# Kernel optimization log

Measured on AMD Instinct MI355X. Metric: run time of the kernel, lower is better.

Reference implementation:

```python
import jax, jax.numpy as jnp
import numpy as np

B = 4096        # batch size
IN = 4096       # in_size
P = 16          # n_partitions
E = IN // P     # embed_dim = 256
EPS = 1e-5
SCALE = np.float32(np.sqrt(E))


def setup_inputs() -> dict:
    key = jax.random.key(0)
    ks = jax.random.split(key, 8)
    rn = lambda k, shape, s=1.0: jax.random.normal(k, shape, dtype=jnp.float32) * s
    return {
        "x": rn(ks[0], (B, IN)),
        "gamma": jnp.ones((IN,), jnp.float32),   # BatchNorm weight
        "beta": jnp.zeros((IN,), jnp.float32),   # BatchNorm bias
        "WQ": rn(ks[1], (E, E), 0.05), "bQ": rn(ks[2], (E,), 0.05),
        "WK": rn(ks[3], (E, E), 0.05), "bK": rn(ks[4], (E,), 0.05),
        "WV": rn(ks[5], (E, E), 0.05), "bV": rn(ks[6], (E,), 0.05),
    }


def reference(x, gamma, beta, WQ, bQ, WK, bK, WV, bV):
    # Training-mode BatchNorm1d over the batch dim (computed once; the torch
    # loop recomputes the identical result n_partitions*3 times).
    mean = jnp.mean(x, axis=0)
    var = jnp.var(x, axis=0)  # biased, as torch BN uses for normalization
    xn = (x - mean) * jax.lax.rsqrt(var + EPS) * gamma + beta

    # Split features into P partitions of size E; shared projections per partition.
    xr = xn.reshape(B, P, E)                      # partition i -> xr[:, i, :]
    Q = xr @ WQ.T + bQ                            # (B, P, E); torch Q[b,e,p] = Q[b,p,e]
    K = xr @ WK.T + bK                            # (B, P, E)
    V = xr @ WV.T + bV                            # (B, P, E)

    # bmm(Q, K^T) with torch layout (B,E,P) x (B,P,E) -> (B,E,E)
    scores = jnp.einsum('bpe,bpf->bef', Q, K) / SCALE
    attn = jax.nn.softmax(scores, axis=2)         # Softmax(dim=2)
    prod = jnp.einsum('bef,bpf->bep', attn, V)    # (B, E, P)

    # torch.cat over embed_dim rows == row-major reshape of (E,P)
    out = prod.reshape(B, E * P) + x
    return out
```

## Files before the change

kernel.cpp:

```cpp
#include <hip/hip_runtime.h>
#include <hip/hip_bf16.h>

#define B_SZ   4096
#define IN_SZ  4096
#define EPS_F  1e-5f
#define CEXP   0.09016844005555896f

typedef __bf16 bf16x8 __attribute__((ext_vector_type(8)));
typedef float  f32x4  __attribute__((ext_vector_type(4)));
typedef float  f32x16 __attribute__((ext_vector_type(16)));

static __device__ __forceinline__ unsigned short f2bf(float f) {
    union { float f; unsigned int u; } c; c.f = f;
    unsigned int u = c.u;
    return (unsigned short)((u + 0x7FFFu + ((u >> 16) & 1u)) >> 16);
}
static __device__ __forceinline__ unsigned short bfbits(float f) {
    __bf16 h = (__bf16)f;
    return __builtin_bit_cast(unsigned short, h);
}
static __device__ __forceinline__ unsigned int pk2(float a, float b) {
    return (unsigned int)bfbits(a) | ((unsigned int)bfbits(b) << 16);
}

__global__ __launch_bounds__(256) void stats_kernel(const float* __restrict__ x,
                                                    float* __restrict__ colsum,
                                                    float* __restrict__ colsq) {
    int c4 = blockIdx.x * 256 + threadIdx.x;
    int r0 = blockIdx.y * 64;
    float4 s = {0.f, 0.f, 0.f, 0.f}, q = {0.f, 0.f, 0.f, 0.f};
    const float4* p = reinterpret_cast<const float4*>(x) + (size_t)r0 * 1024 + c4;
    #pragma unroll 4
    for (int r = 0; r < 64; ++r) {
        float4 v = p[(size_t)r * 1024];
        s.x += v.x; s.y += v.y; s.z += v.z; s.w += v.w;
        q.x += v.x * v.x; q.y += v.y * v.y; q.z += v.z * v.z; q.w += v.w * v.w;
    }
    int j = c4 * 4;
    atomicAdd(&colsum[j + 0], s.x); atomicAdd(&colsum[j + 1], s.y);
    atomicAdd(&colsum[j + 2], s.z); atomicAdd(&colsum[j + 3], s.w);
    atomicAdd(&colsq[j + 0], q.x);  atomicAdd(&colsq[j + 1], q.y);
    atomicAdd(&colsq[j + 2], q.z);  atomicAdd(&colsq[j + 3], q.w);
}

__global__ __launch_bounds__(256) void prep_kernel(const float* __restrict__ gamma,
                                                   const float* __restrict__ beta,
                                                   const float* __restrict__ WQ,
                                                   const float* __restrict__ WK,
                                                   const float* __restrict__ WV,
                                                   const float* __restrict__ colsum,
                                                   const float* __restrict__ colsq,
                                                   float* __restrict__ scale,
                                                   float* __restrict__ shift,
                                                   unsigned short* __restrict__ wbf) {
    int i = blockIdx.x * 256 + threadIdx.x;
    if (i < IN_SZ) {
        float mean = colsum[i] * (1.0f / B_SZ);
        float var  = colsq[i] * (1.0f / B_SZ) - mean * mean;
        float sc   = gamma[i] * rsqrtf(var + EPS_F);
        scale[i] = sc;
        shift[i] = beta[i] - mean * sc;
    }
    wbf[i]           = f2bf(WQ[i]);
    wbf[65536 + i]   = f2bf(WK[i]);
    wbf[131072 + i]  = f2bf(WV[i]);
}

__global__ __launch_bounds__(256, 3) void attn3_kernel(
    const float* __restrict__ x,
    const float* __restrict__ scale,
    const float* __restrict__ shift,
    const unsigned short* __restrict__ wbf,
    const float* __restrict__ bQ,
    const float* __restrict__ bK,
    const float* __restrict__ bV,
    float* __restrict__ out)
{
    __shared__ __align__(16) unsigned short smem[25728];

    const int tid  = threadIdx.x;
    const int lane = tid & 63;
    const int w    = tid >> 6;
    const int b    = blockIdx.x;

    unsigned short* qT  = smem;
    unsigned short* kT  = smem + 6144;
    unsigned short* vS  = smem + 12288;
    unsigned short* xr  = smem + 16512;
    unsigned short* att = smem + 16512 + w * 2304;

    const float* xb = x + (size_t)b * IN_SZ;

    for (int i = tid; i < IN_SZ / 4; i += 256) {
        float4 xv = reinterpret_cast<const float4*>(xb)[i];
        float4 sc = reinterpret_cast<const float4*>(scale)[i];
        float4 sh = reinterpret_cast<const float4*>(shift)[i];
        int j = i * 4;
        int p = j >> 8, f = j & 255;
        unsigned int lo = pk2(xv.x * sc.x + sh.x, xv.y * sc.y + sh.y);
        unsigned int hi = pk2(xv.z * sc.z + sh.z, xv.w * sc.w + sh.w);
        *reinterpret_cast<uint2*>(&xr[p * 264 + f]) = make_uint2(lo, hi);
    }
    __syncthreads();

    const int r16 = lane & 15;
    const int g4  = lane >> 4;
    for (int t = w; t < 48; t += 4) {
        int proj = t >> 4;
        int et   = t & 15;
        const unsigned short* Wg = wbf + proj * 65536 + (et * 16 + r16) * 256 + 8 * g4;
        const unsigned short* arow = &xr[r16 * 264 + 8 * g4];
        f32x4 acc = {0.f, 0.f, 0.f, 0.f};
        #pragma unroll
        for (int kt = 0; kt < 8; ++kt) {
            bf16x8 av = *reinterpret_cast<const bf16x8*>(arow + 32 * kt);
            bf16x8 bv = *reinterpret_cast<const bf16x8*>(Wg + 32 * kt);
            acc = __builtin_amdgcn_mfma_f32_16x16x32_bf16(av, bv, acc, 0, 0, 0);
        }
        const float* bias = (proj == 0) ? bQ : (proj == 1) ? bK : bV;
        float bvv = bias[et * 16 + r16];
        if (proj < 2) {
            unsigned short* dst = (proj == 0 ? qT : kT) + (et * 16 + r16) * 24 + 4 * g4;
            *reinterpret_cast<uint2*>(dst) =
                make_uint2(pk2(acc[0] + bvv, acc[1] + bvv), pk2(acc[2] + bvv, acc[3] + bvv));
        } else {
            #pragma unroll
            for (int i = 0; i < 4; ++i)
                vS[(4 * g4 + i) * 264 + et * 16 + r16] = bfbits(acc[i] + bvv);
        }
    }
    __syncthreads();

    const int c32  = lane & 31;
    const int hi32 = lane >> 5;
    float* ob = out + (size_t)b * IN_SZ;

    for (int et2 = w; et2 < 8; et2 += 4) {
        int e0 = et2 * 32;
        bf16x8 qfrag = *reinterpret_cast<const bf16x8*>(&qT[(e0 + c32) * 24 + 8 * hi32]);
        f32x4 o0 = {0.f, 0.f, 0.f, 0.f}, o1 = {0.f, 0.f, 0.f, 0.f};
        float sum = 0.f;

        #pragma unroll
        for (int fb = 0; fb < 4; ++fb) {
            #pragma unroll
            for (int dd = 0; dd < 2; ++dd) {
                int d = 2 * fb + dd;
                bf16x8 kfrag = *reinterpret_cast<const bf16x8*>(&kT[(32 * d + c32) * 24 + 8 * hi32]);
                f32x16 s;
                #pragma unroll
                for (int r = 0; r < 16; ++r) s[r] = 0.f;
                s = __builtin_amdgcn_mfma_f32_32x32x16_bf16(kfrag, qfrag, s, 0, 0, 0);
                #pragma unroll
                for (int q = 0; q < 4; ++q) {
                    float p0 = exp2f(s[4*q+0] * CEXP);
                    float p1 = exp2f(s[4*q+1] * CEXP);
                    float p2 = exp2f(s[4*q+2] * CEXP);
                    float p3 = exp2f(s[4*q+3] * CEXP);
                    sum += (p0 + p1) + (p2 + p3);
                    *reinterpret_cast<uint2*>(&att[c32 * 72 + dd * 32 + 8 * q + 4 * hi32]) =
                        make_uint2(pk2(p0, p1), pk2(p2, p3));
                }
            }
            #pragma unroll
            for (int kt = 0; kt < 2; ++kt) {
                int fo = 64 * fb + 32 * kt + 8 * g4;
                bf16x8 vfr = *reinterpret_cast<const bf16x8*>(&vS[r16 * 264 + fo]);
                bf16x8 a0  = *reinterpret_cast<const bf16x8*>(&att[r16 * 72 + 32 * kt + 8 * g4]);
                o0 = __builtin_amdgcn_mfma_f32_16x16x32_bf16(a0, vfr, o0, 0, 0, 0);
                bf16x8 a1  = *reinterpret_cast<const bf16x8*>(&att[(16 + r16) * 72 + 32 * kt + 8 * g4]);
                o1 = __builtin_amdgcn_mfma_f32_16x16x32_bf16(a1, vfr, o1, 0, 0, 0);
            }
        }

        sum += __shfl_xor(sum, 32, 64);
        float rinv = 1.0f / sum;
        #pragma unroll
        for (int r = 0; r < 4; ++r) {
            float ri0 = __shfl(rinv, 4 * g4 + r, 64);
            float ri1 = __shfl(rinv, 16 + 4 * g4 + r, 64);
            int j0 = (e0 + 4 * g4 + r) * 16 + r16;
            int j1 = (e0 + 16 + 4 * g4 + r) * 16 + r16;
            ob[j0] = o0[r] * ri0 + xb[j0];
            ob[j1] = o1[r] * ri1 + xb[j1];
        }
    }
}

extern "C" void kernel_launch(void* const* d_in, const int* in_sizes, int n_in,
                              void* d_out, int out_size, void* d_ws, size_t ws_size,
                              hipStream_t stream) {
    (void)in_sizes; (void)n_in; (void)out_size; (void)ws_size;
    const float* x     = (const float*)d_in[0];
    const float* gamma = (const float*)d_in[1];
    const float* beta  = (const float*)d_in[2];
    const float* WQ    = (const float*)d_in[3];
    const float* bQv   = (const float*)d_in[4];
    const float* WK    = (const float*)d_in[5];
    const float* bKv   = (const float*)d_in[6];
    const float* WV    = (const float*)d_in[7];
    const float* bVv   = (const float*)d_in[8];
    float* out = (float*)d_out;

    float* colsum = (float*)d_ws;
    float* colsq  = colsum + 4096;
    float* scale  = colsum + 8192;
    float* shift  = colsum + 12288;
    unsigned short* wbf = (unsigned short*)(colsum + 16384);

    hipMemsetAsync(colsum, 0, 8192 * sizeof(float), stream);
    stats_kernel<<<dim3(4, 64), 256, 0, stream>>>(x, colsum, colsq);
    prep_kernel<<<256, 256, 0, stream>>>(gamma, beta, WQ, WK, WV, colsum, colsq, scale, shift, wbf);
    attn3_kernel<<<4096, 256, 0, stream>>>(x, scale, shift, wbf, bQv, bKv, bVv, out);
}
```

Before: 334.5 us.

## Keep normalized input in registers, swizzle LDS layouts, raise occupancy, fast exp2

Each wave now normalizes its x fragment straight from global memory into registers for the projection MFMAs, so the xr staging buffer in LDS and one barrier go away. The padded LDS layouts for Q, K, V and the attention tile are replaced by dense buffers with XOR swizzles. This shrinks shared memory to 40 KB, allowing launch bounds of 4 blocks per CU. exp2f is also swapped for the hardware exp2 builtin. In exchange, every wave reloads x, scale and shift redundantly (the 4 waves duplicate the same loads), and register pressure is higher under the tighter launch bound.

```diff
diff --git a/kernel.cpp b/kernel.cpp
--- a/kernel.cpp
+++ b/kernel.cpp
@@ -9,6 +9,12 @@
 typedef __bf16 bf16x8 __attribute__((ext_vector_type(8)));
 typedef float  f32x4  __attribute__((ext_vector_type(4)));
 typedef float  f32x16 __attribute__((ext_vector_type(16)));
+
+#if __has_builtin(__builtin_amdgcn_exp2f)
+#define FAST_EXP2(x) __builtin_amdgcn_exp2f(x)
+#else
+#define FAST_EXP2(x) exp2f(x)
+#endif
 
 static __device__ __forceinline__ unsigned short f2bf(float f) {
     union { float f; unsigned int u; } c; c.f = f;
@@ -66,7 +72,7 @@
     wbf[131072 + i]  = f2bf(WV[i]);
 }
 
-__global__ __launch_bounds__(256, 3) void attn3_kernel(
+__global__ __launch_bounds__(256, 4) void attn4_kernel(
     const float* __restrict__ x,
     const float* __restrict__ scale,
     const float* __restrict__ shift,
@@ -76,57 +82,72 @@
     const float* __restrict__ bV,
     float* __restrict__ out)
 {
-    __shared__ __align__(16) unsigned short smem[25728];
+    __shared__ __align__(16) unsigned short smem[20480];
+    char* const base = reinterpret_cast<char*>(smem);
 
     const int tid  = threadIdx.x;
     const int lane = tid & 63;
     const int w    = tid >> 6;
     const int b    = blockIdx.x;
-
-    unsigned short* qT  = smem;
-    unsigned short* kT  = smem + 6144;
-    unsigned short* vS  = smem + 12288;
-    unsigned short* xr  = smem + 16512;
-    unsigned short* att = smem + 16512 + w * 2304;
+    const int r16  = lane & 15;
+    const int g4   = lane >> 4;
+
+    char* const qT  = base;
+    char* const kT  = base + 8192;
+    char* const vS  = base + 16384;
+    char* const att = base + 24576 + w * 4096;
 
     const float* xb = x + (size_t)b * IN_SZ;
 
-    for (int i = tid; i < IN_SZ / 4; i += 256) {
-        float4 xv = reinterpret_cast<const float4*>(xb)[i];
-        float4 sc = reinterpret_cast<const float4*>(scale)[i];
-        float4 sh = reinterpret_cast<const float4*>(shift)[i];
-        int j = i * 4;
-        int p = j >> 8, f = j & 255;
-        unsigned int lo = pk2(xv.x * sc.x + sh.x, xv.y * sc.y + sh.y);
-        unsigned int hi = pk2(xv.z * sc.z + sh.z, xv.w * sc.w + sh.w);
-        *reinterpret_cast<uint2*>(&xr[p * 264 + f]) = make_uint2(lo, hi);
-    }
-    __syncthreads();
-
-    const int r16 = lane & 15;
-    const int g4  = lane >> 4;
+    bf16x8 areg[8];
+    {
+        const float* xr  = xb    + r16 * 256;
+        const float* scr = scale + r16 * 256;
+        const float* shr = shift + r16 * 256;
+        #pragma unroll
+        for (int kt = 0; kt < 8; ++kt) {
+            int c = 8 * g4 + 32 * kt;
+            float4 x0 = *reinterpret_cast<const float4*>(xr + c);
+            float4 x1 = *reinterpret_cast<const float4*>(xr + c + 4);
+            float4 s0 = *reinterpret_cast<const float4*>(scr + c);
+            float4 s1 = *reinterpret_cast<const float4*>(scr + c + 4);
+            float4 h0 = *reinterpret_cast<const float4*>(shr + c);
+            float4 h1 = *reinterpret_cast<const float4*>(shr + c + 4);
+            union { bf16x8 v; unsigned int u[4]; } t;
+            t.u[0] = pk2(fmaf(x0.x, s0.x, h0.x), fmaf(x0.y, s0.y, h0.y));
+            t.u[1] = pk2(fmaf(x0.z, s0.z, h0.z), fmaf(x0.w, s0.w, h0.w));
+            t.u[2] = pk2(fmaf(x1.x, s1.x, h1.x), fmaf(x1.y, s1.y, h1.y));
+            t.u[3] = pk2(fmaf(x1.z, s1.z, h1.z), fmaf(x1.w, s1.w, h1.w));
+            areg[kt] = t.v;
+        }
+    }
+
     for (int t = w; t < 48; t += 4) {
         int proj = t >> 4;
         int et   = t & 15;
         const unsigned short* Wg = wbf + proj * 65536 + (et * 16 + r16) * 256 + 8 * g4;
-        const unsigned short* arow = &xr[r16 * 264 + 8 * g4];
         f32x4 acc = {0.f, 0.f, 0.f, 0.f};
         #pragma unroll
         for (int kt = 0; kt < 8; ++kt) {
-            bf16x8 av = *reinterpret_cast<const bf16x8*>(arow + 32 * kt);
             bf16x8 bv = *reinterpret_cast<const bf16x8*>(Wg + 32 * kt);
-            acc = __builtin_amdgcn_mfma_f32_16x16x32_bf16(av, bv, acc, 0, 0, 0);
+            acc = __builtin_amdgcn_mfma_f32_16x16x32_bf16(areg[kt], bv, acc, 0, 0, 0);
         }
         const float* bias = (proj == 0) ? bQ : (proj == 1) ? bK : bV;
         float bvv = bias[et * 16 + r16];
         if (proj < 2) {
-            unsigned short* dst = (proj == 0 ? qT : kT) + (et * 16 + r16) * 24 + 4 * g4;
-            *reinterpret_cast<uint2*>(dst) =
+            int e = et * 16 + r16;
+            unsigned off = (unsigned)(e * 32 + 8 * g4);
+            off ^= ((off >> 7) & 1u) << 4;
+            *reinterpret_cast<uint2*>((proj == 0 ? qT : kT) + off) =
                 make_uint2(pk2(acc[0] + bvv, acc[1] + bvv), pk2(acc[2] + bvv, acc[3] + bvv));
         } else {
             #pragma unroll
-            for (int i = 0; i < 4; ++i)
-                vS[(4 * g4 + i) * 264 + et * 16 + r16] = bfbits(acc[i] + bvv);
+            for (int i = 0; i < 4; ++i) {
+                int p = 4 * g4 + i;
+                unsigned off = (unsigned)(p * 512 + (et * 16 + r16) * 2);
+                off ^= ((off >> 9) & 7u) << 4;
+                *reinterpret_cast<unsigned short*>(vS + off) = bfbits(acc[i] + bvv);
+            }
         }
     }
     __syncthreads();
@@ -137,7 +158,9 @@
 
     for (int et2 = w; et2 < 8; et2 += 4) {
         int e0 = et2 * 32;
-        bf16x8 qfrag = *reinterpret_cast<const bf16x8*>(&qT[(e0 + c32) * 24 + 8 * hi32]);
+        unsigned qoff = (unsigned)((e0 + c32) * 32 + 16 * hi32);
+        qoff ^= ((qoff >> 7) & 1u) << 4;
+        bf16x8 qfrag = *reinterpret_cast<const bf16x8*>(qT + qoff);
         f32x4 o0 = {0.f, 0.f, 0.f, 0.f}, o1 = {0.f, 0.f, 0.f, 0.f};
         float sum = 0.f;
 
@@ -146,29 +169,37 @@
             #pragma unroll
             for (int dd = 0; dd < 2; ++dd) {
                 int d = 2 * fb + dd;
-                bf16x8 kfrag = *reinterpret_cast<const bf16x8*>(&kT[(32 * d + c32) * 24 + 8 * hi32]);
+                unsigned koff = (unsigned)((32 * d + c32) * 32 + 16 * hi32);
+                koff ^= ((koff >> 7) & 1u) << 4;
+                bf16x8 kfrag = *reinterpret_cast<const bf16x8*>(kT + koff);
                 f32x16 s;
                 #pragma unroll
                 for (int r = 0; r < 16; ++r) s[r] = 0.f;
                 s = __builtin_amdgcn_mfma_f32_32x32x16_bf16(kfrag, qfrag, s, 0, 0, 0);
                 #pragma unroll
                 for (int q = 0; q < 4; ++q) {
-                    float p0 = exp2f(s[4*q+0] * CEXP);
-                    float p1 = exp2f(s[4*q+1] * CEXP);
-                    float p2 = exp2f(s[4*q+2] * CEXP);
-                    float p3 = exp2f(s[4*q+3] * CEXP);
+                    float p0 = FAST_EXP2(s[4*q+0] * CEXP);
+                    float p1 = FAST_EXP2(s[4*q+1] * CEXP);
+                    float p2 = FAST_EXP2(s[4*q+2] * CEXP);
+                    float p3 = FAST_EXP2(s[4*q+3] * CEXP);
                     sum += (p0 + p1) + (p2 + p3);
-                    *reinterpret_cast<uint2*>(&att[c32 * 72 + dd * 32 + 8 * q + 4 * hi32]) =
-                        make_uint2(pk2(p0, p1), pk2(p2, p3));
+                    unsigned aoff = (unsigned)(c32 * 128 + dd * 64 + 16 * q + 8 * hi32);
+                    aoff ^= ((aoff >> 7) & 7u) << 4;
+                    *reinterpret_cast<uint2*>(att + aoff) = make_uint2(pk2(p0, p1), pk2(p2, p3));
                 }
             }
             #pragma unroll
-            for (int kt = 0; kt < 2; ++kt) {
-                int fo = 64 * fb + 32 * kt + 8 * g4;
-                bf16x8 vfr = *reinterpret_cast<const bf16x8*>(&vS[r16 * 264 + fo]);
-                bf16x8 a0  = *reinterpret_cast<const bf16x8*>(&att[r16 * 72 + 32 * kt + 8 * g4]);
+            for (int kt2 = 0; kt2 < 2; ++kt2) {
+                unsigned voff = (unsigned)(r16 * 512 + fb * 128 + kt2 * 64 + g4 * 16);
+                voff ^= ((voff >> 9) & 7u) << 4;
+                bf16x8 vfr = *reinterpret_cast<const bf16x8*>(vS + voff);
+                unsigned a0off = (unsigned)(r16 * 128 + kt2 * 64 + g4 * 16);
+                a0off ^= ((a0off >> 7) & 7u) << 4;
+                bf16x8 a0 = *reinterpret_cast<const bf16x8*>(att + a0off);
                 o0 = __builtin_amdgcn_mfma_f32_16x16x32_bf16(a0, vfr, o0, 0, 0, 0);
-                bf16x8 a1  = *reinterpret_cast<const bf16x8*>(&att[(16 + r16) * 72 + 32 * kt + 8 * g4]);
+                unsigned a1off = (unsigned)((16 + r16) * 128 + kt2 * 64 + g4 * 16);
+                a1off ^= ((a1off >> 7) & 7u) << 4;
+                bf16x8 a1 = *reinterpret_cast<const bf16x8*>(att + a1off);
                 o1 = __builtin_amdgcn_mfma_f32_16x16x32_bf16(a1, vfr, o1, 0, 0, 0);
             }
         }
@@ -211,5 +242,5 @@
     hipMemsetAsync(colsum, 0, 8192 * sizeof(float), stream);
     stats_kernel<<<dim3(4, 64), 256, 0, stream>>>(x, colsum, colsq);
     prep_kernel<<<256, 256, 0, stream>>>(gamma, beta, WQ, WK, WV, colsum, colsq, scale, shift, wbf);
-    attn3_kernel<<<4096, 256, 0, stream>>>(x, scale, shift, wbf, bQv, bKv, bVv, out);
-}
+    attn4_kernel<<<4096, 256, 0, stream>>>(x, scale, shift, wbf, bQv, bKv, bVv, out);
+}
```

Result: slower. 393.3 us (+17.6%).
